# Optimization experiments

Hardware: AMD Instinct MI355X
Metric: run time of the kernel (lower is better)

## Reference

```python
import jax, jax.numpy as jnp
import numpy as np

B, INPUT_DIM, HEAD = 16384, 1024, 8
DIM = INPUT_DIM // HEAD


def setup_inputs() -> dict:
    key = jax.random.key(0)
    k1, k2, kw1, kb1, kw2, kw3 = jax.random.split(key, 6)
    x1 = jax.random.normal(k1, (B, INPUT_DIM), dtype=jnp.float32)
    x2 = jax.random.normal(k2, (B, INPUT_DIM), dtype=jnp.float32)
    s = 1.0 / np.sqrt(DIM)
    W1 = jax.random.uniform(kw1, (HEAD, DIM), jnp.float32, -s, s)   # per-head Linear(dim,1) weight
    b1 = jax.random.uniform(kb1, (HEAD,), jnp.float32, -s, s)       # per-head Linear(dim,1) bias
    W2 = jax.random.uniform(kw2, (HEAD, DIM), jnp.float32, -s, s)   # per-head Linear(dim,1,bias=False)
    W3 = jax.random.uniform(kw3, (HEAD, DIM, DIM), jnp.float32, -s, s)  # per-head Linear(dim,dim) [out,in]
    return {"x1": x1, "x2": x2, "W1": W1, "b1": b1, "W2": W2, "W3": W3}


def reference(x1, x2, W1, b1, W2, W3):
    b = x1.shape[0]
    h1 = x1.reshape(b, HEAD, DIM)
    h2 = x2.reshape(b, HEAD, DIM)
    # per-head scalar linears: [b, head]
    t1 = jnp.einsum('bhd,hd->bh', h1, W1) + b1
    t2 = jnp.einsum('bhd,hd->bh', h2, W2)
    # diag(w3(x1_h) @ x2_h^T) == sum((x1_h @ W3_h^T) * x2_h, -1), batched over heads
    proj = jnp.einsum('bhi,hoi->bho', h1, W3)
    t3 = jnp.sum(proj * h2, axis=-1)
    return jnp.sum(t1 + t2 + t3, axis=1)  # [b]
```

## Files before the change

kernel.cpp:

```cpp
#include <hip/hip_runtime.h>


#define NB 16384
#define NHEAD 8
#define NDIM 128

typedef __attribute__((ext_vector_type(8))) short bf16x8;
typedef __attribute__((ext_vector_type(16))) float f32x16;

__device__ __forceinline__ void gload_lds16(const void* g, void* l) {
    __builtin_amdgcn_global_load_lds(
        (const __attribute__((address_space(1))) unsigned*)g,
        (__attribute__((address_space(3))) unsigned*)l, 16, 0, 0);
}

__global__ __launch_bounds__(256) void prep_w3(
    const float* __restrict__ W3, short* __restrict__ whi,
    short* __restrict__ wlo)
{
    const int t    = blockIdx.x * 256 + threadIdx.x;
    const int lane = t & 63;
    const int nt   = (t >> 6) & 3;
    const int ks   = (t >> 8) & 7;
    const int h    = t >> 11;
    const int n    = nt * 32 + (lane & 31);
    const int k    = ks * 16 + (lane >> 5) * 8;

    const float* src = W3 + ((size_t)(h * NDIM + n)) * NDIM + k;
    const float4 a = *reinterpret_cast<const float4*>(src);
    const float4 b = *reinterpret_cast<const float4*>(src + 4);
    float xf[8] = {a.x, a.y, a.z, a.w, b.x, b.y, b.z, b.w};
    bf16x8 hi, lo;
#pragma unroll
    for (int j = 0; j < 8; ++j) {
        const unsigned u = __float_as_uint(xf[j]);
        hi[j] = (short)(u >> 16);
        const float hf = __uint_as_float(u & 0xffff0000u);
        lo[j] = (short)(__float_as_uint(xf[j] - hf) >> 16);
    }
    reinterpret_cast<bf16x8*>(whi)[t] = hi;
    reinterpret_cast<bf16x8*>(wlo)[t] = lo;
}

__global__ __launch_bounds__(256, 4) void bilinear_mfma(
    const float* __restrict__ x1, const float* __restrict__ x2,
    const float* __restrict__ W1, const float* __restrict__ W2,
    const short* __restrict__ whi, const short* __restrict__ wlo,
    float* __restrict__ psum)
{
    const int tid  = threadIdx.x;
    const int w    = tid >> 6;
    const int l    = tid & 63;
    const int col  = l & 31;
    const int hi5  = l >> 5;
    const int bid  = blockIdx.x;
    const int h    = bid & 7;
    const int bw   = (bid >> 3) * 128 + w * 32;

    __shared__ short lhi[4][4][512];
    __shared__ short llo[4][4][512];

    const short* __restrict__ shi = whi + (size_t)h * 16384;
    const short* __restrict__ slo = wlo + (size_t)h * 16384;
    const float* __restrict__ w1base = W1 + h * NDIM;
    const float* __restrict__ x1row  = x1 + (size_t)(bw + col) * (NHEAD * NDIM)
                                          + h * NDIM + hi5 * 8;

    f32x16 acc[4];
#pragma unroll
    for (int nt = 0; nt < 4; ++nt) acc[nt] = (f32x16)0.f;
    float t1 = 0.f;

    for (int p = 0; p < 2; ++p) {
#pragma unroll
        for (int i = 0; i < 4; ++i) {
            gload_lds16(shi + (size_t)(p * 1024 + i * 256 + tid) * 8,
                        &lhi[0][0][0] + (size_t)(i * 256 + w * 64) * 8);
            gload_lds16(slo + (size_t)(p * 1024 + i * 256 + tid) * 8,
                        &llo[0][0][0] + (size_t)(i * 256 + w * 64) * 8);
        }
        __syncthreads();

#pragma unroll
        for (int ks = 0; ks < 4; ++ks) {
            const int kbase = p * 64 + ks * 16;

            bf16x8 ahi, alo;
            {
                const float4 a = *reinterpret_cast<const float4*>(x1row + kbase);
                const float4 b = *reinterpret_cast<const float4*>(x1row + kbase + 4);
                float xf[8] = {a.x, a.y, a.z, a.w, b.x, b.y, b.z, b.w};
#pragma unroll
                for (int j = 0; j < 8; ++j) {
                    const float w1l = w1base[kbase + j];
                    const float w1h = w1base[kbase + 8 + j];
                    const unsigned u = __float_as_uint(xf[j]);
                    ahi[j] = (short)(u >> 16);
                    alo[j] = (short)(__float_as_uint(
                        xf[j] - __uint_as_float(u & 0xffff0000u)) >> 16);
                    t1 += xf[j] * (hi5 ? w1h : w1l);
                }
            }

#pragma unroll
            for (int nt = 0; nt < 4; ++nt) {
                const bf16x8 bhi = *reinterpret_cast<const bf16x8*>(&lhi[ks][nt][l * 8]);
                const bf16x8 blo = *reinterpret_cast<const bf16x8*>(&llo[ks][nt][l * 8]);
                acc[nt] = __builtin_amdgcn_mfma_f32_32x32x16_bf16(ahi, bhi, acc[nt], 0, 0, 0);
                acc[nt] = __builtin_amdgcn_mfma_f32_32x32x16_bf16(alo, bhi, acc[nt], 0, 0, 0);
                acc[nt] = __builtin_amdgcn_mfma_f32_32x32x16_bf16(ahi, blo, acc[nt], 0, 0, 0);
            }
        }
        if (p == 0) __syncthreads();
    }

    float w2v[4];
#pragma unroll
    for (int nt = 0; nt < 4; ++nt) w2v[nt] = W2[h * NDIM + nt * 32 + col];

    float cr[16];
#pragma unroll
    for (int reg = 0; reg < 16; ++reg) {
        const int row = (reg & 3) + 8 * (reg >> 2) + 4 * hi5;
        const float* x2p = x2 + (size_t)(bw + row) * (NHEAD * NDIM)
                              + h * NDIM + col;
        float s = 0.f;
#pragma unroll
        for (int nt = 0; nt < 4; ++nt)
            s += (acc[nt][reg] + w2v[nt]) * x2p[nt * 32];
        cr[reg] = s;
    }
#pragma unroll
    for (int m = 1; m < 32; m <<= 1)
#pragma unroll
        for (int reg = 0; reg < 16; ++reg)
            cr[reg] += __shfl_xor(cr[reg], m, 64);

    float tf = t1;
    tf += __shfl_xor(tf, 32, 64);
#pragma unroll
    for (int reg = 0; reg < 16; ++reg) {
        const int row = (reg & 3) + 8 * (reg >> 2) + 4 * hi5;
        cr[reg] += __shfl(tf, row, 64);
    }

    float outv = cr[0];
#pragma unroll
    for (int reg = 1; reg < 16; ++reg)
        if (col == reg) outv = cr[reg];
    if (col < 16) {
        const int row = (col & 3) + 8 * (col >> 2) + 4 * hi5;
        psum[(size_t)h * NB + bw + row] = outv;
    }
}

__global__ __launch_bounds__(256) void bilinear_reduce(
    const float* __restrict__ psum, const float* __restrict__ b1,
    float* __restrict__ out)
{
    const int i = blockIdx.x * 256 + threadIdx.x;
    float bs = 0.f;
#pragma unroll
    for (int hh = 0; hh < NHEAD; ++hh) bs += b1[hh];
    float s = bs;
#pragma unroll
    for (int hh = 0; hh < NHEAD; ++hh) s += psum[(size_t)hh * NB + i];
    out[i] = s;
}

extern "C" void kernel_launch(void* const* d_in, const int* in_sizes, int n_in,
                              void* d_out, int out_size, void* d_ws, size_t ws_size,
                              hipStream_t stream) {
    const float* x1 = (const float*)d_in[0];
    const float* x2 = (const float*)d_in[1];
    const float* W1 = (const float*)d_in[2];
    const float* b1 = (const float*)d_in[3];
    const float* W2 = (const float*)d_in[4];
    const float* W3 = (const float*)d_in[5];
    float* out = (float*)d_out;

    short* whi = (short*)d_ws;
    short* wlo = whi + (size_t)NHEAD * NDIM * NDIM;
    float* psum = (float*)((char*)d_ws + 512 * 1024);

    prep_w3<<<dim3(64), dim3(256), 0, stream>>>(W3, whi, wlo);
    bilinear_mfma<<<dim3(NB / 128 * NHEAD), dim3(256), 0, stream>>>(
        x1, x2, W1, W2, whi, wlo, psum);
    bilinear_reduce<<<dim3(NB / 256), dim3(256), 0, stream>>>(psum, b1, out);
}
```

Before: 37.64 us.

## Fuse W3 split, bilinear MFMA and head reduction into one kernel

Removes the separate W3 bf16 hi/lo prep kernel and the per-head partial-sum reduction kernel. Each block now converts its head's full W3 slice to hi/lo bf16 directly into shared memory, covers 256 rows with 512 threads, and atomically adds its per-head result plus bias into a zeroed output. This cuts two kernel launches and the psum round trip through memory. In exchange every block redoes the W3 conversion from fp32 global memory, uses twice the LDS, and adds a memset and eight-way atomic contention per output.

```diff
diff --git a/kernel.cpp b/kernel.cpp
--- a/kernel.cpp
+++ b/kernel.cpp
@@ -8,60 +8,48 @@
 typedef __attribute__((ext_vector_type(8))) short bf16x8;
 typedef __attribute__((ext_vector_type(16))) float f32x16;
 
-__device__ __forceinline__ void gload_lds16(const void* g, void* l) {
-    __builtin_amdgcn_global_load_lds(
-        (const __attribute__((address_space(1))) unsigned*)g,
-        (__attribute__((address_space(3))) unsigned*)l, 16, 0, 0);
-}
-
-__global__ __launch_bounds__(256) void prep_w3(
-    const float* __restrict__ W3, short* __restrict__ whi,
-    short* __restrict__ wlo)
+__global__ __launch_bounds__(512, 4) void bilinear_fused(
+    const float* __restrict__ x1, const float* __restrict__ x2,
+    const float* __restrict__ W1, const float* __restrict__ b1,
+    const float* __restrict__ W2, const float* __restrict__ W3,
+    float* __restrict__ out)
 {
-    const int t    = blockIdx.x * 256 + threadIdx.x;
-    const int lane = t & 63;
-    const int nt   = (t >> 6) & 3;
-    const int ks   = (t >> 8) & 7;
-    const int h    = t >> 11;
-    const int n    = nt * 32 + (lane & 31);
-    const int k    = ks * 16 + (lane >> 5) * 8;
-
-    const float* src = W3 + ((size_t)(h * NDIM + n)) * NDIM + k;
-    const float4 a = *reinterpret_cast<const float4*>(src);
-    const float4 b = *reinterpret_cast<const float4*>(src + 4);
-    float xf[8] = {a.x, a.y, a.z, a.w, b.x, b.y, b.z, b.w};
-    bf16x8 hi, lo;
-#pragma unroll
-    for (int j = 0; j < 8; ++j) {
-        const unsigned u = __float_as_uint(xf[j]);
-        hi[j] = (short)(u >> 16);
-        const float hf = __uint_as_float(u & 0xffff0000u);
-        lo[j] = (short)(__float_as_uint(xf[j] - hf) >> 16);
-    }
-    reinterpret_cast<bf16x8*>(whi)[t] = hi;
-    reinterpret_cast<bf16x8*>(wlo)[t] = lo;
-}
-
-__global__ __launch_bounds__(256, 4) void bilinear_mfma(
-    const float* __restrict__ x1, const float* __restrict__ x2,
-    const float* __restrict__ W1, const float* __restrict__ W2,
-    const short* __restrict__ whi, const short* __restrict__ wlo,
-    float* __restrict__ psum)
-{
-    const int tid  = threadIdx.x;
+    const int tid = threadIdx.x;
+    const int bid = blockIdx.x;
     const int w    = tid >> 6;
     const int l    = tid & 63;
     const int col  = l & 31;
     const int hi5  = l >> 5;
-    const int bid  = blockIdx.x;
     const int h    = bid & 7;
-    const int bw   = (bid >> 3) * 128 + w * 32;
+    const int bw   = (bid >> 3) * 256 + w * 32;
 
-    __shared__ short lhi[4][4][512];
-    __shared__ short llo[4][4][512];
+    __shared__ short lhi[8][4][512];
+    __shared__ short llo[8][4][512];
 
-    const short* __restrict__ shi = whi + (size_t)h * 16384;
-    const short* __restrict__ slo = wlo + (size_t)h * 16384;
+#pragma unroll
+    for (int i = 0; i < 4; ++i) {
+        const int s    = i * 512 + tid;
+        const int lane = s & 63;
+        const int nt   = (s >> 6) & 3;
+        const int ks   = s >> 8;
+        const int n    = nt * 32 + (lane & 31);
+        const int k    = ks * 16 + (lane >> 5) * 8;
+        const float* src = W3 + ((size_t)(h * NDIM + n)) * NDIM + k;
+        const float4 a = *reinterpret_cast<const float4*>(src);
+        const float4 b = *reinterpret_cast<const float4*>(src + 4);
+        float xf[8] = {a.x, a.y, a.z, a.w, b.x, b.y, b.z, b.w};
+        bf16x8 hi, lo;
+#pragma unroll
+        for (int j = 0; j < 8; ++j) {
+            const unsigned u = __float_as_uint(xf[j]);
+            hi[j] = (short)(u >> 16);
+            const float hf = __uint_as_float(u & 0xffff0000u);
+            lo[j] = (short)(__float_as_uint(xf[j] - hf) >> 16);
+        }
+        *reinterpret_cast<bf16x8*>(&lhi[ks][nt][lane * 8]) = hi;
+        *reinterpret_cast<bf16x8*>(&llo[ks][nt][lane * 8]) = lo;
+    }
+
     const float* __restrict__ w1base = W1 + h * NDIM;
     const float* __restrict__ x1row  = x1 + (size_t)(bw + col) * (NHEAD * NDIM)
                                           + h * NDIM + hi5 * 8;
@@ -71,47 +59,37 @@
     for (int nt = 0; nt < 4; ++nt) acc[nt] = (f32x16)0.f;
     float t1 = 0.f;
 
-    for (int p = 0; p < 2; ++p) {
-#pragma unroll
-        for (int i = 0; i < 4; ++i) {
-            gload_lds16(shi + (size_t)(p * 1024 + i * 256 + tid) * 8,
-                        &lhi[0][0][0] + (size_t)(i * 256 + w * 64) * 8);
-            gload_lds16(slo + (size_t)(p * 1024 + i * 256 + tid) * 8,
-                        &llo[0][0][0] + (size_t)(i * 256 + w * 64) * 8);
-        }
-        __syncthreads();
+    __syncthreads();
 
 #pragma unroll
-        for (int ks = 0; ks < 4; ++ks) {
-            const int kbase = p * 64 + ks * 16;
+    for (int ks = 0; ks < 8; ++ks) {
+        const int kbase = ks * 16;
 
-            bf16x8 ahi, alo;
-            {
-                const float4 a = *reinterpret_cast<const float4*>(x1row + kbase);
-                const float4 b = *reinterpret_cast<const float4*>(x1row + kbase + 4);
-                float xf[8] = {a.x, a.y, a.z, a.w, b.x, b.y, b.z, b.w};
+        bf16x8 ahi, alo;
+        {
+            const float4 a = *reinterpret_cast<const float4*>(x1row + kbase);
+            const float4 b = *reinterpret_cast<const float4*>(x1row + kbase + 4);
+            float xf[8] = {a.x, a.y, a.z, a.w, b.x, b.y, b.z, b.w};
 #pragma unroll
-                for (int j = 0; j < 8; ++j) {
-                    const float w1l = w1base[kbase + j];
-                    const float w1h = w1base[kbase + 8 + j];
-                    const unsigned u = __float_as_uint(xf[j]);
-                    ahi[j] = (short)(u >> 16);
-                    alo[j] = (short)(__float_as_uint(
-                        xf[j] - __uint_as_float(u & 0xffff0000u)) >> 16);
-                    t1 += xf[j] * (hi5 ? w1h : w1l);
-                }
+            for (int j = 0; j < 8; ++j) {
+                const float w1l = w1base[kbase + j];
+                const float w1h = w1base[kbase + 8 + j];
+                const unsigned u = __float_as_uint(xf[j]);
+                ahi[j] = (short)(u >> 16);
+                alo[j] = (short)(__float_as_uint(
+                    xf[j] - __uint_as_float(u & 0xffff0000u)) >> 16);
+                t1 += xf[j] * (hi5 ? w1h : w1l);
             }
+        }
 
 #pragma unroll
-            for (int nt = 0; nt < 4; ++nt) {
-                const bf16x8 bhi = *reinterpret_cast<const bf16x8*>(&lhi[ks][nt][l * 8]);
-                const bf16x8 blo = *reinterpret_cast<const bf16x8*>(&llo[ks][nt][l * 8]);
-                acc[nt] = __builtin_amdgcn_mfma_f32_32x32x16_bf16(ahi, bhi, acc[nt], 0, 0, 0);
-                acc[nt] = __builtin_amdgcn_mfma_f32_32x32x16_bf16(alo, bhi, acc[nt], 0, 0, 0);
-                acc[nt] = __builtin_amdgcn_mfma_f32_32x32x16_bf16(ahi, blo, acc[nt], 0, 0, 0);
-            }
+        for (int nt = 0; nt < 4; ++nt) {
+            const bf16x8 bhi = *reinterpret_cast<const bf16x8*>(&lhi[ks][nt][l * 8]);
+            const bf16x8 blo = *reinterpret_cast<const bf16x8*>(&llo[ks][nt][l * 8]);
+            acc[nt] = __builtin_amdgcn_mfma_f32_32x32x16_bf16(ahi, bhi, acc[nt], 0, 0, 0);
+            acc[nt] = __builtin_amdgcn_mfma_f32_32x32x16_bf16(alo, bhi, acc[nt], 0, 0, 0);
+            acc[nt] = __builtin_amdgcn_mfma_f32_32x32x16_bf16(ahi, blo, acc[nt], 0, 0, 0);
         }
-        if (p == 0) __syncthreads();
     }
 
     float w2v[4];
@@ -150,22 +128,8 @@
         if (col == reg) outv = cr[reg];
     if (col < 16) {
         const int row = (col & 3) + 8 * (col >> 2) + 4 * hi5;
-        psum[(size_t)h * NB + bw + row] = outv;
+        atomicAdd(&out[bw + row], outv + b1[h]);
     }
-}
-
-__global__ __launch_bounds__(256) void bilinear_reduce(
-    const float* __restrict__ psum, const float* __restrict__ b1,
-    float* __restrict__ out)
-{
-    const int i = blockIdx.x * 256 + threadIdx.x;
-    float bs = 0.f;
-#pragma unroll
-    for (int hh = 0; hh < NHEAD; ++hh) bs += b1[hh];
-    float s = bs;
-#pragma unroll
-    for (int hh = 0; hh < NHEAD; ++hh) s += psum[(size_t)hh * NB + i];
-    out[i] = s;
 }
 
 extern "C" void kernel_launch(void* const* d_in, const int* in_sizes, int n_in,
@@ -179,12 +143,7 @@
     const float* W3 = (const float*)d_in[5];
     float* out = (float*)d_out;
 
-    short* whi = (short*)d_ws;
-    short* wlo = whi + (size_t)NHEAD * NDIM * NDIM;
-    float* psum = (float*)((char*)d_ws + 512 * 1024);
-
-    prep_w3<<<dim3(64), dim3(256), 0, stream>>>(W3, whi, wlo);
-    bilinear_mfma<<<dim3(NB / 128 * NHEAD), dim3(256), 0, stream>>>(
-        x1, x2, W1, W2, whi, wlo, psum);
-    bilinear_reduce<<<dim3(NB / 256), dim3(256), 0, stream>>>(psum, b1, out);
+    hipMemsetAsync(out, 0, (size_t)NB * sizeof(float), stream);
+    bilinear_fused<<<dim3(NB / 256 * NHEAD), dim3(512), 0, stream>>>(
+        x1, x2, W1, b1, W2, W3, out);
 }
```

After: 43.83 us. +16.4%, slower.
